# Kernel optimization log

Measured on AMD Instinct MI355X. Metric: run time of the kernel, lower is better.

## Reference

```python
import jax, jax.numpy as jnp
import numpy as np

B, L, D = 2, 1024, 768
NH, HD = 12, 64
NL = 6
MLP = 3072
THETA = 10000.0


def _rope(pos, dim, theta):
    # pos: (L,) float -> (L, dim//2, 2, 2) rotation matrices (FLUX rope)
    omega = 1.0 / (theta ** (jnp.arange(0, dim, 2, dtype=jnp.float32) / dim))
    out = pos[:, None] * omega  # (L, dim//2)
    cos, sin = jnp.cos(out), jnp.sin(out)
    return jnp.stack([jnp.stack([cos, -sin], -1), jnp.stack([sin, cos], -1)], -2)


def _build_pe(seq_len, pe_dim):
    # 2D spatial ids: axis0 = x (fast), axis1 = y (slow); axes_dim = [pe_dim//2, pe_dim//2]
    h = w = int(seq_len ** 0.5)
    y_ids = jnp.repeat(jnp.arange(h, dtype=jnp.float32), w)
    x_ids = jnp.tile(jnp.arange(w, dtype=jnp.float32), h)
    half = pe_dim // 2
    pe = jnp.concatenate([_rope(x_ids, half, THETA), _rope(y_ids, half, THETA)], axis=-3)
    return pe[None, None]  # (1, 1, L, pe_dim//2, 2, 2)


def _apply_rope(x, pe):
    # x: (B, H, L, HD)
    xs = x.reshape(x.shape[:-1] + (-1, 1, 2))
    out = pe[..., 0] * xs[..., 0] + pe[..., 1] * xs[..., 1]
    return out.reshape(x.shape)


def _rmsnorm(x, scale):
    return x * jax.lax.rsqrt(jnp.mean(x * x, axis=-1, keepdims=True) + 1e-6) * scale


def _layernorm(x, g, b):
    m = jnp.mean(x, axis=-1, keepdims=True)
    v = jnp.var(x, axis=-1, keepdims=True)
    return (x - m) * jax.lax.rsqrt(v + 1e-5) * g + b


def _forward(spatial_features, density_weights, condition_embeddings,
             spatial_w, spatial_b, cond_w, cond_b,
             ln1_g, ln1_b, qkv_w, q_scale, k_scale, proj_w, proj_b,
             dscale, dbias, ln2_g, ln2_b, mlp_w1, mlp_b1, mlp_w2, mlp_b2,
             out_w, out_b):
    Bsz, Ls, Ds = spatial_features.shape
    x = spatial_features @ spatial_w + spatial_b
    x = x + (condition_embeddings @ cond_w + cond_b)[:, None, :]
    pe = _build_pe(Ls, HD)
    dflat = density_weights.reshape(Bsz, 1, Ls)  # H*W == L, no interpolation
    attn_scale = HD ** -0.5
    for i in range(NL):
        h = _layernorm(x, ln1_g[i], ln1_b[i])
        qkv = (h @ qkv_w[i]).reshape(Bsz, Ls, 3, NH, HD).transpose(2, 0, 3, 1, 4)
        q, k, v = qkv[0], qkv[1], qkv[2]
        q = _rmsnorm(q, q_scale[i])
        k = _rmsnorm(k, k_scale[i])
        q = _apply_rope(q, pe)
        k = _apply_rope(k, pe)
        scores = jnp.einsum('bhld,bhmd->bhlm', q, k) * attn_scale
        scores = scores + (dscale[i] * dflat[..., None] + dbias[i])  # (B,1,L,1) bcast
        attn = jax.nn.softmax(scores, axis=-1)
        o = jnp.einsum('bhlm,bhmd->bhld', attn, v)
        o = o.transpose(0, 2, 1, 3).reshape(Bsz, Ls, Ds)
        x = x + o @ proj_w[i] + proj_b[i]
        h2 = _layernorm(x, ln2_g[i], ln2_b[i])
        x = x + jax.nn.gelu(h2 @ mlp_w1[i] + mlp_b1[i], approximate=False) @ mlp_w2[i] + mlp_b2[i]
    return x @ out_w + out_b


def setup_inputs() -> dict:
    key = jax.random.key(0)
    ks = jax.random.split(key, 16)
    s = 0.02
    inp = {
        'spatial_features': jax.random.normal(ks[0], (B, L, D), jnp.float32),
        'density_weights': jax.random.uniform(ks[1], (B, 32, 32), jnp.float32),
        'condition_embeddings': jax.random.normal(ks[2], (B, 1536), jnp.float32),
        'spatial_w': jax.random.normal(ks[3], (D, D), jnp.float32) * s,
        'spatial_b': jnp.zeros((D,), jnp.float32),
        'cond_w': jax.random.normal(ks[4], (1536, D), jnp.float32) * s,
        'cond_b': jnp.zeros((D,), jnp.float32),
        'ln1_g': jnp.ones((NL, D), jnp.float32),
        'ln1_b': jnp.zeros((NL, D), jnp.float32),
        'qkv_w': jax.random.normal(ks[5], (NL, D, 3 * D), jnp.float32) * s,
        'q_scale': jnp.ones((NL, HD), jnp.float32),
        'k_scale': jnp.ones((NL, HD), jnp.float32),
        'proj_w': jax.random.normal(ks[6], (NL, D, D), jnp.float32) * s,
        'proj_b': jnp.zeros((NL, D), jnp.float32),
        'dscale': jnp.ones((NL,), jnp.float32),
        'dbias': jnp.zeros((NL,), jnp.float32),
        'ln2_g': jnp.ones((NL, D), jnp.float32),
        'ln2_b': jnp.zeros((NL, D), jnp.float32),
        'mlp_w1': jax.random.normal(ks[7], (NL, D, MLP), jnp.float32) * s,
        'mlp_b1': jnp.zeros((NL, MLP), jnp.float32),
        'mlp_w2': jax.random.normal(ks[8], (NL, MLP, D), jnp.float32) * s,
        'mlp_b2': jnp.zeros((NL, D), jnp.float32),
        'out_w': jax.random.normal(ks[9], (D, D), jnp.float32) * s,
        'out_b': jnp.zeros((D,), jnp.float32),
    }
    return inp


def reference(spatial_features, density_weights, condition_embeddings,
              spatial_w, spatial_b, cond_w, cond_b,
              ln1_g, ln1_b, qkv_w, q_scale, k_scale, proj_w, proj_b,
              dscale, dbias, ln2_g, ln2_b, mlp_w1, mlp_b1, mlp_w2, mlp_b2,
              out_w, out_b):
    return _forward(spatial_features, density_weights, condition_embeddings,
                    spatial_w, spatial_b, cond_w, cond_b,
                    ln1_g, ln1_b, qkv_w, q_scale, k_scale, proj_w, proj_b,
                    dscale, dbias, ln2_g, ln2_b, mlp_w1, mlp_b1, mlp_w2, mlp_b2,
                    out_w, out_b)
```

## Files before the change

### kernel.cpp

```cpp
#include <hip/hip_runtime.h>
#include <hip/hip_bf16.h>
#include <cstdint>
#include <cstddef>

typedef unsigned short u16;
using short8  = __attribute__((ext_vector_type(8))) short;
using floatx4 = __attribute__((ext_vector_type(4))) float;

typedef __attribute__((address_space(1))) void gvoid;
typedef __attribute__((address_space(3))) void svoid;

__device__ __forceinline__ u16 f2bf(float f) {
  __hip_bfloat16 h = __float2bfloat16(f);
  return __builtin_bit_cast(u16, h);
}

__device__ __forceinline__ floatx4 mfma16(short8 a, short8 b, floatx4 c) {
  return __builtin_amdgcn_mfma_f32_16x16x32_bf16(a, b, c, 0, 0, 0);
}

__device__ __forceinline__ void glds16(const u16* g, u16* l) {
  __builtin_amdgcn_global_load_lds((gvoid*)g, (svoid*)l, 16, 0, 0);
}

__global__ void pe_kernel(float* __restrict__ pet) {
  int t = blockIdx.x * 256 + threadIdx.x;
  if (t >= 32768) return;
  int l = t >> 5, j = t & 31;
  float pos   = (j < 16) ? (float)(l & 31) : (float)(l >> 5);
  float omega = powf(10000.f, -(float)(j & 15) / 16.f);
  float a = pos * omega;
  pet[2 * t]     = cosf(a);
  pet[2 * t + 1] = sinf(a);
}

__global__ __launch_bounds__(256) void twt_kernel(const float* __restrict__ in,
                                                  u16* __restrict__ out, int K, int N) {
  size_t lofs = (size_t)blockIdx.z * K * N;
  in  += lofs;
  out += lofs;
  __shared__ float tile[32][33];
  int bx = blockIdx.x;
  int by = blockIdx.y;
  int tx = threadIdx.x & 31, ty = threadIdx.x >> 5;
  #pragma unroll
  for (int p = 0; p < 4; p++) {
    int k = by * 32 + ty + p * 8;
    tile[ty + p * 8][tx] = in[(size_t)k * N + bx * 32 + tx];
  }
  __syncthreads();
  #pragma unroll
  for (int p = 0; p < 4; p++) {
    int n = bx * 32 + ty + p * 8;
    out[(size_t)n * K + by * 32 + tx] = f2bf(tile[tx][ty + p * 8]);
  }
}

__global__ void cvt_kernel(const float* __restrict__ in, u16* __restrict__ out, int n) {
  int i = blockIdx.x * 256 + threadIdx.x;
  if (i < n) out[i] = f2bf(in[i]);
}

__global__ __launch_bounds__(256) void condp_kernel(const float* __restrict__ ce,
                                                    const float* __restrict__ w,
                                                    float* __restrict__ partial) {
  int d = blockIdx.x * 256 + threadIdx.x;
  int c = blockIdx.y;
  #pragma unroll
  for (int b = 0; b < 2; b++) {
    float acc = 0.f;
    #pragma unroll 4
    for (int k = c * 96; k < c * 96 + 96; k++) acc += ce[b * 1536 + k] * w[(size_t)k * 768 + d];
    partial[(size_t)(c * 2 + b) * 768 + d] = acc;
  }
}

__global__ __launch_bounds__(256) void condr_kernel(const float* __restrict__ partial,
                                                    const float* __restrict__ bias,
                                                    float* __restrict__ out) {
  int t = blockIdx.x * 256 + threadIdx.x;
  int b = t / 768, d = t % 768;
  float acc = bias[d];
  #pragma unroll
  for (int c = 0; c < 16; c++) acc += partial[(size_t)(c * 2 + b) * 768 + d];
  out[b * 768 + d] = acc;
}

__global__ __launch_bounds__(256) void ln_kernel(const float* __restrict__ x,
                                                 const float* __restrict__ g,
                                                 const float* __restrict__ b,
                                                 u16* __restrict__ out) {
  int row = blockIdx.x;
  const float* xr = x + (size_t)row * 768;
  int t = threadIdx.x;
  float v0 = xr[t], v1 = xr[t + 256], v2 = xr[t + 512];
  float s = v0 + v1 + v2, s2 = v0 * v0 + v1 * v1 + v2 * v2;
  #pragma unroll
  for (int o = 32; o >= 1; o >>= 1) { s += __shfl_xor(s, o); s2 += __shfl_xor(s2, o); }
  __shared__ float red[8];
  int w = t >> 6, lane = t & 63;
  if (lane == 0) { red[w] = s; red[4 + w] = s2; }
  __syncthreads();
  s  = red[0] + red[1] + red[2] + red[3];
  s2 = red[4] + red[5] + red[6] + red[7];
  float mean = s * (1.f / 768.f);
  float var  = s2 * (1.f / 768.f) - mean * mean;
  float rstd = rsqrtf(var + 1e-5f);
  u16* orow = out + (size_t)row * 768;
  orow[t]       = f2bf((v0 - mean) * rstd * g[t] + b[t]);
  orow[t + 256] = f2bf((v1 - mean) * rstd * g[t + 256] + b[t + 256]);
  orow[t + 512] = f2bf((v2 - mean) * rstd * g[t + 512] + b[t + 512]);
}

__global__ __launch_bounds__(256) void ropeq_kernel(const float* __restrict__ qkv,
                                                    const float* __restrict__ qs,
                                                    const float* __restrict__ ks,
                                                    const float* __restrict__ pet,
                                                    u16* __restrict__ qb, u16* __restrict__ kb) {
  int gid = blockIdx.x * 4 + (threadIdx.x >> 6);
  int lane = threadIdx.x & 63;
  int h = gid % 12, bl = gid / 12;
  int l = bl & 1023, b = bl >> 10;
  const float* qp = qkv + ((size_t)(b * 1024 + l) * 3 + 0) * 768 + h * 64;
  const float* kp = qp + 768;
  float q = qp[lane], k = kp[lane];
  float sq = q * q, sk = k * k;
  #pragma unroll
  for (int o = 1; o < 64; o <<= 1) { sq += __shfl_xor(sq, o); sk += __shfl_xor(sk, o); }
  q *= rsqrtf(sq * (1.f / 64.f) + 1e-6f) * qs[lane];
  k *= rsqrtf(sk * (1.f / 64.f) + 1e-6f) * ks[lane];
  int j = lane >> 1;
  float c = pet[(l * 32 + j) * 2], s = pet[(l * 32 + j) * 2 + 1];
  float qo = __shfl_xor(q, 1), ko = __shfl_xor(k, 1);
  float qr = (lane & 1) ? (s * qo + c * q) : (c * q - s * qo);
  float kr = (lane & 1) ? (s * ko + c * k) : (c * k - s * ko);
  int bh = b * 12 + h;
  qb[((size_t)bh * 1024 + l) * 64 + lane] = f2bf(qr * 0.125f);
  kb[((size_t)bh * 1024 + l) * 64 + lane] = f2bf(kr);
}

__global__ __launch_bounds__(256) void vtrans_kernel(const float* __restrict__ qkv,
                                                     u16* __restrict__ vt) {
  int lt = blockIdx.x, bh = blockIdx.y;
  int b = bh / 12, h = bh % 12;
  __shared__ float tile[64][65];
  int t = threadIdx.x, c = t & 63, r0 = t >> 6;
  #pragma unroll
  for (int p = 0; p < 16; p++) {
    int lr = p * 4 + r0;
    tile[lr][c] = qkv[((size_t)(b * 1024 + lt * 64 + lr) * 3 + 2) * 768 + h * 64 + c];
  }
  __syncthreads();
  #pragma unroll
  for (int p = 0; p < 16; p++) {
    int d = p * 4 + r0;
    vt[((size_t)bh * 64 + d) * 1024 + lt * 64 + c] = f2bf(tile[c][d]);
  }
}

__global__ __launch_bounds__(256) void attn_split(const u16* __restrict__ qb,
                                                  const u16* __restrict__ kbuf,
                                                  const u16* __restrict__ vt,
                                                  float* __restrict__ po,
                                                  float* __restrict__ pl) {
  const int qt = blockIdx.x, bh = blockIdx.y, sp = blockIdx.z;
  const int lane = threadIdx.x & 63, w = threadIdx.x >> 6;
  const int quad = lane >> 4, l16 = lane & 15;
  __shared__ __align__(16) u16 Ks[128 * 64];
  __shared__ __align__(16) u16 Vs[64 * 128];
  __shared__ __align__(16) u16 Ps[4][16 * 136];
  const u16* Q  = qb   + (size_t)bh * 1024 * 64;
  const u16* Kp = kbuf + (size_t)bh * 1024 * 64;
  const u16* Vp = vt   + (size_t)bh * 64 * 1024;
  const int qrow0 = qt * 64 + w * 16;
  short8 aq0, aq1;
  {
    const u16* qp = Q + (size_t)(qrow0 + l16) * 64 + quad * 8;
    aq0 = *(const short8*)qp;
    aq1 = *(const short8*)(qp + 32);
  }
  floatx4 accO[4];
  #pragma unroll
  for (int i = 0; i < 4; i++) accO[i] = (floatx4){0.f, 0.f, 0.f, 0.f};
  float lsum[4] = {0.f, 0.f, 0.f, 0.f};

  const int krow_in = (lane >> 3);
  const int kchunk  = lane & 7;
  const int vrow_in = (lane >> 4);
  const int vchunk  = lane & 15;

  for (int nt = 0; nt < 4; ++nt) {
    const int kb0 = sp * 512 + nt * 128;
    __syncthreads();
    #pragma unroll
    for (int j = 0; j < 4; j++) {
      int r = w * 32 + j * 8 + krow_in;
      int g = kchunk ^ (r & 7);
      glds16(Kp + (size_t)(kb0 + r) * 64 + g * 8, Ks + (w * 32 + j * 8) * 64);
    }
    #pragma unroll
    for (int j = 0; j < 4; j++) {
      int r = w * 16 + j * 4 + vrow_in;
      int g = vchunk ^ (r & 15);
      glds16(Vp + (size_t)r * 1024 + kb0 + g * 8, Vs + (w * 16 + j * 4) * 128);
    }
    __syncthreads();

    floatx4 s[8];
    #pragma unroll
    for (int n = 0; n < 8; n++) {
      int row = n * 16 + l16;
      int c0 = quad ^ (l16 & 7);
      short8 b0 = *(const short8*)&Ks[row * 64 + c0 * 8];
      short8 b1 = *(const short8*)&Ks[row * 64 + (c0 ^ 4) * 8];
      floatx4 z = (floatx4){0.f, 0.f, 0.f, 0.f};
      z = mfma16(aq0, b0, z);
      s[n] = mfma16(aq1, b1, z);
    }
    #pragma unroll
    for (int n = 0; n < 8; n++) {
      #pragma unroll
      for (int r = 0; r < 4; r++) {
        float pv = __expf(s[n][r] - 8.f);
        lsum[r] += pv;
        Ps[w][(quad * 4 + r) * 136 + n * 16 + l16] = f2bf(pv);
      }
    }
    #pragma unroll
    for (int kt = 0; kt < 4; kt++) {
      short8 ap = *(const short8*)&Ps[w][l16 * 136 + kt * 32 + quad * 8];
      #pragma unroll
      for (int dt = 0; dt < 4; dt++) {
        int vrow = dt * 16 + l16;
        int c = (kt * 4 + quad) ^ l16;
        short8 bv = *(const short8*)&Vs[vrow * 128 + c * 8];
        accO[dt] = mfma16(ap, bv, accO[dt]);
      }
    }
  }
  #pragma unroll
  for (int r = 0; r < 4; r++) {
    #pragma unroll
    for (int o = 1; o < 16; o <<= 1) lsum[r] += __shfl_xor(lsum[r], o);
  }
  const size_t sb = (size_t)(sp * 24 + bh) * 1024;
  #pragma unroll
  for (int r = 0; r < 4; r++) {
    int lr = qrow0 + quad * 4 + r;
    if (l16 == 0) pl[sb + lr] = lsum[r];
    #pragma unroll
    for (int dt = 0; dt < 4; dt++)
      po[(sb + lr) * 64 + dt * 16 + l16] = accO[dt][r];
  }
}

__global__ __launch_bounds__(256) void attn_comb(const float* __restrict__ po,
                                                 const float* __restrict__ pl,
                                                 u16* __restrict__ obuf) {
  int w = threadIdx.x >> 6, lane = threadIdx.x & 63;
  int gr = blockIdx.x * 4 + w;
  int bh = gr >> 10, l = gr & 1023;
  float num = 0.f, den = 0.f;
  #pragma unroll
  for (int s = 0; s < 2; s++) {
    num += po[((size_t)(s * 24 + bh) * 1024 + l) * 64 + lane];
    den += pl[(size_t)(s * 24 + bh) * 1024 + l];
  }
  int b = bh / 12, h = bh % 12;
  obuf[((size_t)(b * 1024 + l)) * 768 + h * 64 + lane] = f2bf(num / den);
}

template <int EPI, int BN>
__global__ __launch_bounds__(256) void gemm_bt(const u16* __restrict__ A,
                                               const u16* __restrict__ Bt,
                                               const float* __restrict__ bias,
                                               const float* extra,
                                               float* Cf, u16* Cb, int M, int N, int K) {
  constexpr int ROWS = 64 + BN;
  constexpr int LDW  = 72;
  constexpr int NCH  = ROWS * 8 / 256;
  constexpr int NTW  = BN / 32;
  __shared__ __align__(16) u16 S[2][ROWS * LDW];
  const int t = threadIdx.x;
  const int lane = t & 63, w = t >> 6;
  const int quad = lane >> 4, l16 = lane & 15;
  const int m0 = blockIdx.y * 64, n0 = blockIdx.x * BN;
  const int wm = (w >> 1) * 32, wn = (w & 1) * (BN / 2);
  floatx4 acc[2][NTW];
  #pragma unroll
  for (int i = 0; i < 2; i++)
    #pragma unroll
    for (int j = 0; j < NTW; j++) acc[i][j] = (floatx4){0.f, 0.f, 0.f, 0.f};

  const u16* gsrc[NCH];
  int laddr[NCH];
  #pragma unroll
  for (int j = 0; j < NCH; j++) {
    int idx = j * 256 + t;
    int row = idx >> 3, c = idx & 7;
    const u16* base = (row < 64) ? (A + (size_t)(m0 + row) * K)
                                 : (Bt + (size_t)(n0 + row - 64) * K);
    gsrc[j] = base + c * 8;
    laddr[j] = row * LDW + c * 8;
  }
  short8 stg0[NCH], stg1[NCH];

  const int NIT = K / 64;

  #pragma unroll
  for (int j = 0; j < NCH; j++) stg0[j] = *(const short8*)(gsrc[j]);
  #pragma unroll
  for (int j = 0; j < NCH; j++) stg1[j] = *(const short8*)(gsrc[j] + 64);
  #pragma unroll
  for (int j = 0; j < NCH; j++) *(short8*)&S[0][laddr[j]] = stg0[j];
  __syncthreads();

  auto compute = [&](int buf) {
    #pragma unroll
    for (int kk = 0; kk < 2; kk++) {
      short8 af[2], bfr[NTW];
      #pragma unroll
      for (int mt = 0; mt < 2; mt++)
        af[mt] = *(const short8*)&S[buf][(wm + mt * 16 + l16) * LDW + kk * 32 + quad * 8];
      #pragma unroll
      for (int nt = 0; nt < NTW; nt++)
        bfr[nt] = *(const short8*)&S[buf][(64 + wn + nt * 16 + l16) * LDW + kk * 32 + quad * 8];
      #pragma unroll
      for (int mt = 0; mt < 2; mt++)
        #pragma unroll
        for (int nt = 0; nt < NTW; nt++)
          acc[mt][nt] = mfma16(af[mt], bfr[nt], acc[mt][nt]);
    }
  };

  for (int it = 0; it < NIT; it += 2) {
    if (it + 2 < NIT) {
      #pragma unroll
      for (int j = 0; j < NCH; j++) stg0[j] = *(const short8*)(gsrc[j] + (it + 2) * 64);
    }
    compute(0);
    #pragma unroll
    for (int j = 0; j < NCH; j++) *(short8*)&S[1][laddr[j]] = stg1[j];
    __syncthreads();
    if (it + 3 < NIT) {
      #pragma unroll
      for (int j = 0; j < NCH; j++) stg1[j] = *(const short8*)(gsrc[j] + (it + 3) * 64);
    }
    compute(1);
    if (it + 2 < NIT) {
      #pragma unroll
      for (int j = 0; j < NCH; j++) *(short8*)&S[0][laddr[j]] = stg0[j];
    }
    __syncthreads();
  }

  #pragma unroll
  for (int mt = 0; mt < 2; mt++) {
    #pragma unroll
    for (int nt = 0; nt < NTW; nt++) {
      int col = n0 + wn + nt * 16 + l16;
      float bcol = bias ? bias[col] : 0.f;
      #pragma unroll
      for (int r = 0; r < 4; r++) {
        int row = m0 + wm + mt * 16 + quad * 4 + r;
        float v = acc[mt][nt][r] + bcol;
        if (EPI == 1) v += extra[(row >> 10) * N + col];
        if (EPI == 2) v += extra[(size_t)row * N + col];
        if (EPI == 3) v = 0.5f * v * (1.f + erff(v * 0.70710678118654752f));
        if (Cf) Cf[(size_t)row * N + col] = v;
        if (Cb) Cb[(size_t)row * N + col] = f2bf(v);
      }
    }
  }
}

extern "C" void kernel_launch(void* const* d_in, const int* in_sizes, int n_in,
                              void* d_out, int out_size, void* d_ws, size_t ws_size,
                              hipStream_t stream) {
  const float* sf   = (const float*)d_in[0];
  const float* ce   = (const float*)d_in[2];
  const float* sw   = (const float*)d_in[3];
  const float* sb   = (const float*)d_in[4];
  const float* cw   = (const float*)d_in[5];
  const float* cb   = (const float*)d_in[6];
  const float* ln1g = (const float*)d_in[7];
  const float* ln1b = (const float*)d_in[8];
  const float* qkvw = (const float*)d_in[9];
  const float* qsc  = (const float*)d_in[10];
  const float* ksc  = (const float*)d_in[11];
  const float* pw   = (const float*)d_in[12];
  const float* pb   = (const float*)d_in[13];
  const float* ln2g = (const float*)d_in[16];
  const float* ln2b = (const float*)d_in[17];
  const float* w1   = (const float*)d_in[18];
  const float* b1   = (const float*)d_in[19];
  const float* w2   = (const float*)d_in[20];
  const float* b2   = (const float*)d_in[21];
  const float* ow   = (const float*)d_in[22];
  const float* ob   = (const float*)d_in[23];

  char* p = (char*)d_ws;
  auto alloc = [&](size_t bytes) { char* r = p; p += (bytes + 255) & ~(size_t)255; return r; };
  float* pet  = (float*)alloc((size_t)1024 * 32 * 2 * 4);
  u16* swT    = (u16*)alloc((size_t)768 * 768 * 2);
  u16* owT    = (u16*)alloc((size_t)768 * 768 * 2);
  u16* qkvT   = (u16*)alloc((size_t)6 * 2304 * 768 * 2);
  u16* pwT    = (u16*)alloc((size_t)6 * 768 * 768 * 2);
  u16* w1T    = (u16*)alloc((size_t)6 * 3072 * 768 * 2);
  u16* w2T    = (u16*)alloc((size_t)6 * 768 * 3072 * 2);
  u16* sfb    = (u16*)alloc((size_t)2048 * 768 * 2);
  float* cpar = (float*)alloc((size_t)32 * 768 * 4);
  float* cond = (float*)alloc((size_t)2 * 768 * 4);
  float* x    = (float*)alloc((size_t)2048 * 768 * 4);
  u16* xb     = (u16*)alloc((size_t)2048 * 768 * 2);
  u16* h      = (u16*)alloc((size_t)2048 * 768 * 2);
  float* qkv  = (float*)alloc((size_t)2048 * 2304 * 4);
  u16* qbuf   = (u16*)alloc((size_t)2048 * 768 * 2);
  u16* kbuf   = (u16*)alloc((size_t)2048 * 768 * 2);
  u16* vtb    = (u16*)alloc((size_t)2048 * 768 * 2);
  u16* obuf   = (u16*)alloc((size_t)2048 * 768 * 2);
  u16* gbuf   = (u16*)alloc((size_t)2048 * 3072 * 2);
  float* po   = (float*)alloc((size_t)2 * 24 * 1024 * 64 * 4);
  float* pl   = (float*)alloc((size_t)2 * 24 * 1024 * 4);

  pe_kernel<<<128, 256, 0, stream>>>(pet);
  twt_kernel<<<dim3(24, 24, 1), 256, 0, stream>>>(sw, swT, 768, 768);
  twt_kernel<<<dim3(24, 24, 1), 256, 0, stream>>>(ow, owT, 768, 768);
  twt_kernel<<<dim3(72, 24, 6), 256, 0, stream>>>(qkvw, qkvT, 768, 2304);
  twt_kernel<<<dim3(24, 24, 6), 256, 0, stream>>>(pw, pwT, 768, 768);
  twt_kernel<<<dim3(96, 24, 6), 256, 0, stream>>>(w1, w1T, 768, 3072);
  twt_kernel<<<dim3(24, 96, 6), 256, 0, stream>>>(w2, w2T, 3072, 768);
  cvt_kernel<<<(2048 * 768) / 256, 256, 0, stream>>>(sf, sfb, 2048 * 768);
  condp_kernel<<<dim3(3, 16), 256, 0, stream>>>(ce, cw, cpar);
  condr_kernel<<<6, 256, 0, stream>>>(cpar, cb, cond);

  gemm_bt<1, 64><<<dim3(12, 32), 256, 0, stream>>>(sfb, swT, sb, cond, x, nullptr, 2048, 768, 768);

  for (int i = 0; i < 6; i++) {
    ln_kernel<<<2048, 256, 0, stream>>>(x, ln1g + i * 768, ln1b + i * 768, h);
    gemm_bt<0, 128><<<dim3(18, 32), 256, 0, stream>>>(h, qkvT + (size_t)i * 2304 * 768,
                                                      nullptr, nullptr, qkv, nullptr, 2048, 2304, 768);
    ropeq_kernel<<<6144, 256, 0, stream>>>(qkv, qsc + i * 64, ksc + i * 64, pet, qbuf, kbuf);
    vtrans_kernel<<<dim3(16, 24), 256, 0, stream>>>(qkv, vtb);
    attn_split<<<dim3(16, 24, 2), 256, 0, stream>>>(qbuf, kbuf, vtb, po, pl);
    attn_comb<<<6144, 256, 0, stream>>>(po, pl, obuf);
    gemm_bt<2, 64><<<dim3(12, 32), 256, 0, stream>>>(obuf, pwT + (size_t)i * 768 * 768,
                                                     pb + i * 768, x, x, xb, 2048, 768, 768);
    ln_kernel<<<2048, 256, 0, stream>>>(x, ln2g + i * 768, ln2b + i * 768, h);
    gemm_bt<3, 128><<<dim3(24, 32), 256, 0, stream>>>(h, w1T + (size_t)i * 3072 * 768,
                                                      b1 + i * 3072, nullptr, nullptr, gbuf, 2048, 3072, 768);
    gemm_bt<2, 64><<<dim3(12, 32), 256, 0, stream>>>(gbuf, w2T + (size_t)i * 768 * 3072,
                                                     b2 + i * 768, x, x, xb, 2048, 768, 3072);
  }
  gemm_bt<0, 64><<<dim3(12, 32), 256, 0, stream>>>(xb, owT, ob, nullptr, (float*)d_out, nullptr,
                                                   2048, 768, 768);
}
```

Before: 1.126 ms.

## Load GEMM tiles directly into LDS with XOR-swizzled layout

The GEMM kernel stops staging tiles through registers and stores them to LDS with global_load_lds instead, which removes the register-to-LDS copy and the VGPR pressure of the staging arrays. Padded rows are replaced by an unpadded 64-wide layout with an XOR swizzle on 16-byte chunks to avoid bank conflicts. The software pipeline becomes a simple double buffer with one barrier per iteration. The direct-to-LDS loads rely on vmcnt and the barrier for ordering, and the lane-contiguous destination pattern limits how the swizzle can be applied.

```diff
diff --git a/kernel.cpp b/kernel.cpp
--- a/kernel.cpp
+++ b/kernel.cpp
@@ -277,54 +277,51 @@
                                                const float* extra,
                                                float* Cf, u16* Cb, int M, int N, int K) {
   constexpr int ROWS = 64 + BN;
-  constexpr int LDW  = 72;
-  constexpr int NCH  = ROWS * 8 / 256;
+  constexpr int RPW  = ROWS / 4;
+  constexpr int NG   = RPW / 8;
   constexpr int NTW  = BN / 32;
-  __shared__ __align__(16) u16 S[2][ROWS * LDW];
+  __shared__ __align__(16) u16 S[2][ROWS * 64];
   const int t = threadIdx.x;
   const int lane = t & 63, w = t >> 6;
   const int quad = lane >> 4, l16 = lane & 15;
   const int m0 = blockIdx.y * 64, n0 = blockIdx.x * BN;
   const int wm = (w >> 1) * 32, wn = (w & 1) * (BN / 2);
+
   floatx4 acc[2][NTW];
   #pragma unroll
   for (int i = 0; i < 2; i++)
     #pragma unroll
     for (int j = 0; j < NTW; j++) acc[i][j] = (floatx4){0.f, 0.f, 0.f, 0.f};
 
-  const u16* gsrc[NCH];
-  int laddr[NCH];
-  #pragma unroll
-  for (int j = 0; j < NCH; j++) {
-    int idx = j * 256 + t;
-    int row = idx >> 3, c = idx & 7;
-    const u16* base = (row < 64) ? (A + (size_t)(m0 + row) * K)
-                                 : (Bt + (size_t)(n0 + row - 64) * K);
-    gsrc[j] = base + c * 8;
-    laddr[j] = row * LDW + c * 8;
-  }
-  short8 stg0[NCH], stg1[NCH];
-
-  const int NIT = K / 64;
-
-  #pragma unroll
-  for (int j = 0; j < NCH; j++) stg0[j] = *(const short8*)(gsrc[j]);
-  #pragma unroll
-  for (int j = 0; j < NCH; j++) stg1[j] = *(const short8*)(gsrc[j] + 64);
-  #pragma unroll
-  for (int j = 0; j < NCH; j++) *(short8*)&S[0][laddr[j]] = stg0[j];
-  __syncthreads();
+  const u16* gsrc[NG];
+  int loff[NG];
+  #pragma unroll
+  for (int j = 0; j < NG; j++) {
+    int r = w * RPW + j * 8 + (lane >> 3);
+    int c = lane & 7;
+    int g = c ^ (r & 7);
+    const u16* base = (r < 64) ? (A + (size_t)(m0 + r) * K)
+                               : (Bt + (size_t)(n0 + r - 64) * K);
+    gsrc[j] = base + g * 8;
+    loff[j] = (w * RPW + j * 8) * 64;
+  }
+
+  const int NIT = K >> 6;
 
   auto compute = [&](int buf) {
     #pragma unroll
     for (int kk = 0; kk < 2; kk++) {
       short8 af[2], bfr[NTW];
       #pragma unroll
-      for (int mt = 0; mt < 2; mt++)
-        af[mt] = *(const short8*)&S[buf][(wm + mt * 16 + l16) * LDW + kk * 32 + quad * 8];
-      #pragma unroll
-      for (int nt = 0; nt < NTW; nt++)
-        bfr[nt] = *(const short8*)&S[buf][(64 + wn + nt * 16 + l16) * LDW + kk * 32 + quad * 8];
+      for (int mt = 0; mt < 2; mt++) {
+        int ra = wm + mt * 16 + l16;
+        af[mt] = *(const short8*)&S[buf][ra * 64 + ((((kk << 2) | quad)) ^ (ra & 7)) * 8];
+      }
+      #pragma unroll
+      for (int nt = 0; nt < NTW; nt++) {
+        int rb = 64 + wn + nt * 16 + l16;
+        bfr[nt] = *(const short8*)&S[buf][rb * 64 + ((((kk << 2) | quad)) ^ (rb & 7)) * 8];
+      }
       #pragma unroll
       for (int mt = 0; mt < 2; mt++)
         #pragma unroll
@@ -333,26 +330,19 @@
     }
   };
 
-  for (int it = 0; it < NIT; it += 2) {
-    if (it + 2 < NIT) {
-      #pragma unroll
-      for (int j = 0; j < NCH; j++) stg0[j] = *(const short8*)(gsrc[j] + (it + 2) * 64);
-    }
-    compute(0);
-    #pragma unroll
-    for (int j = 0; j < NCH; j++) *(short8*)&S[1][laddr[j]] = stg1[j];
+  #pragma unroll
+  for (int j = 0; j < NG; j++) glds16(gsrc[j], &S[0][loff[j]]);
+  __syncthreads();
+
+  int cur = 0;
+  for (int it = 1; it < NIT; ++it) {
+    #pragma unroll
+    for (int j = 0; j < NG; j++) glds16(gsrc[j] + it * 64, &S[cur ^ 1][loff[j]]);
+    compute(cur);
     __syncthreads();
-    if (it + 3 < NIT) {
-      #pragma unroll
-      for (int j = 0; j < NCH; j++) stg1[j] = *(const short8*)(gsrc[j] + (it + 3) * 64);
-    }
-    compute(1);
-    if (it + 2 < NIT) {
-      #pragma unroll
-      for (int j = 0; j < NCH; j++) *(short8*)&S[0][laddr[j]] = stg0[j];
-    }
-    __syncthreads();
-  }
+    cur ^= 1;
+  }
+  compute(cur);
 
   #pragma unroll
   for (int mt = 0; mt < 2; mt++) {
```

New measurement: 1.028 ms. 1.09x faster.
